# Kernel tuning notes

Measured on AMD Instinct MI355X. Metric: run time of the kernel, lower is better.

The kernel has to match this reference:

```python
import jax, jax.numpy as jnp
import numpy as np

K_MASK = -2.3819763e38  # gemma masking constant


def apply_rope(inputs, positions, head_dim):
    # inputs: [B, T, N, H], positions: [B, T]
    half = head_dim // 2
    fraction = 2.0 * jnp.arange(half, dtype=jnp.float32) / head_dim
    timescale = 10000.0 ** fraction                      # [half]
    sinusoid = positions[..., None].astype(jnp.float32) / timescale  # [B, T, half]
    sin = jnp.sin(sinusoid)[:, :, None, :]               # [B, T, 1, half]
    cos = jnp.cos(sinusoid)[:, :, None, :]
    first, second = jnp.split(inputs, 2, axis=-1)
    out = jnp.concatenate([first * cos - second * sin,
                           second * cos + first * sin], axis=-1)
    return out.astype(inputs.dtype)


def setup_inputs() -> dict:
    key = jax.random.key(0)
    k0, k1, k2, k3 = jax.random.split(key, 4)
    B, T, D, N, H = 4, 1024, 2048, 16, 128
    x = jax.random.normal(k0, (B, T, D), dtype=jnp.float32)
    wq = jax.random.normal(k1, (N, D, H), dtype=jnp.float32) * 0.02
    wkv = jax.random.normal(k2, (2, 1, D, H), dtype=jnp.float32) * 0.02  # MQA: 1 kv head
    wo = jax.random.normal(k3, (N, H, D), dtype=jnp.float32) * 0.02
    segment_pos = jnp.broadcast_to(jnp.arange(T, dtype=jnp.int32), (B, T))
    attn_mask = jnp.broadcast_to(jnp.tril(jnp.ones((T, T), dtype=bool)), (B, T, T))
    return {"x": x, "wq": wq, "wkv": wkv, "wo": wo,
            "segment_pos": segment_pos, "attn_mask": attn_mask}


def reference(x, wq, wkv, wo, segment_pos, attn_mask):
    N, _, H = wq.shape
    # projections
    q = jnp.einsum('BTD,NDH->BTNH', x, wq)          # [B,T,N,H]
    kv = jnp.einsum('BSD,CKDH->CBSKH', x, wkv)      # [2,B,S,1,H]
    k, v = kv[0], kv[1]
    # RoPE + scaling
    q = apply_rope(q, segment_pos, H) * (H ** -0.5)
    k = apply_rope(k, segment_pos, H)
    # MQA head repeat: 1 kv head -> N heads
    k = jnp.repeat(k, N, axis=-2)                   # [B,S,N,H]
    v = jnp.repeat(v, N, axis=-2)
    # attention with manual masked softmax
    logits = jnp.einsum('BTNH,BSNH->BTNS', q, k)
    padded = jnp.where(attn_mask[:, :, None, :], logits, K_MASK)
    probs = jax.nn.softmax(padded, axis=-1).astype(k.dtype)
    encoded = jnp.einsum('BTNS,BSNH->BTNH', probs, v)
    return jnp.einsum('BTNH,NHD->BTD', encoded, wo)
```

## Files before the change

kernel.cpp:

```cpp
#include <hip/hip_runtime.h>
#include <cstdint>
#include <cstddef>

typedef unsigned short u16;
typedef __attribute__((ext_vector_type(8))) short bf16x8;
typedef __attribute__((ext_vector_type(4))) float f32x4;

#define B_ 4
#define T_ 1024
#define D_ 2048
#define N_ 16
#define H_ 128
#define BT_ (B_ * T_)
#define KMASK (-2.3819763e38f)

__device__ __forceinline__ u16 f2bf(float f) {
  uint32_t u = __builtin_bit_cast(uint32_t, f);
  u += 0x7FFFu + ((u >> 16) & 1u);
  return (u16)(u >> 16);
}
__device__ __forceinline__ float bf2f(uint32_t u) {
  return __builtin_bit_cast(float, u << 16);
}

__device__ __forceinline__ void gload16(const void* g, void* l) {
  __builtin_amdgcn_global_load_lds((const __attribute__((address_space(1))) void*)g,
                                   (__attribute__((address_space(3))) void*)l, 16, 0, 0);
}

__global__ __launch_bounds__(256) void convert_x_kernel(const float* __restrict__ x,
                                                        u16* __restrict__ xb) {
  int i = (blockIdx.x * 256 + threadIdx.x) * 8;
  float4 v0 = *(const float4*)(x + i);
  float4 v1 = *(const float4*)(x + i + 4);
  uint4 o;
  o.x = (uint32_t)f2bf(v0.x) | ((uint32_t)f2bf(v0.y) << 16);
  o.y = (uint32_t)f2bf(v0.z) | ((uint32_t)f2bf(v0.w) << 16);
  o.z = (uint32_t)f2bf(v1.x) | ((uint32_t)f2bf(v1.y) << 16);
  o.w = (uint32_t)f2bf(v1.z) | ((uint32_t)f2bf(v1.w) << 16);
  *(uint4*)(xb + i) = o;
}

__global__ __launch_bounds__(256) void transpose_kernel(const float* __restrict__ src,
                                                        u16* __restrict__ dst, int R, int C) {
  __shared__ float tile[32][33];
  const int z = blockIdx.z;
  const float* s = src + (size_t)z * R * C;
  u16* d = dst + (size_t)z * R * C;
  const int tx = threadIdx.x, ty = threadIdx.y;
  const int r0 = blockIdx.y * 32, c0 = blockIdx.x * 32;
#pragma unroll
  for (int i = 0; i < 4; ++i)
    tile[ty + i * 8][tx] = s[(size_t)(r0 + ty + i * 8) * C + (c0 + tx)];
  __syncthreads();
#pragma unroll
  for (int i = 0; i < 4; ++i)
    d[(size_t)(c0 + ty + i * 8) * R + (r0 + tx)] = f2bf(tile[tx][ty + i * 8]);
}

__global__ __launch_bounds__(256) void rope_table_kernel(float* __restrict__ costab,
                                                         float* __restrict__ sintab) {
  int idx = blockIdx.x * 256 + threadIdx.x;
  int p = idx >> 6, i = idx & 63;
  float ts = powf(10000.0f, (float)i * (1.0f / 64.0f));
  float ang = (float)p / ts;
  costab[idx] = cosf(ang);
  sintab[idx] = sinf(ang);
}

__global__ __launch_bounds__(256) void proj_gemm_kernel(
    const u16* __restrict__ xb, const u16* __restrict__ wqT, const u16* __restrict__ wkvT,
    u16* __restrict__ qraw, u16* __restrict__ kraw, u16* __restrict__ vT) {
  __shared__ alignas(16) u16 a_lds[128 * 64];
  __shared__ alignas(16) u16 b_lds[128 * 64];
  const int bid = blockIdx.x;
  const int newbid = (bid & 7) * 72 + (bid >> 3);
  const int y = newbid >> 5;
  const int m0 = (newbid & 31) * 128;
  const u16* Bt = (y < N_) ? (wqT + (size_t)y * H_ * D_) : (wkvT + (size_t)(y - N_) * H_ * D_);
  const int tid = threadIdx.x;
  const int w = tid >> 6, lane = tid & 63;
  const int g = lane >> 4, li = lane & 15;
  const int mrow = (w >> 1) * 64, wc = (w & 1) * 64;
  f32x4 acc[4][4];
#pragma unroll
  for (int i = 0; i < 4; ++i)
#pragma unroll
    for (int j = 0; j < 4; ++j) acc[i][j] = (f32x4){0.f, 0.f, 0.f, 0.f};

  for (int k0 = 0; k0 < D_; k0 += 64) {
    __syncthreads();
#pragma unroll
    for (int it = 0; it < 4; ++it) {
      int chunk = it * 256 + tid;
      int row = chunk >> 3, cu = chunk & 7;
      gload16(xb + (size_t)(m0 + row) * D_ + k0 + ((cu ^ (row & 7)) << 3), &a_lds[chunk * 8]);
    }
#pragma unroll
    for (int it = 0; it < 4; ++it) {
      int chunk = it * 256 + tid;
      int row = chunk >> 3, cu = chunk & 7;
      gload16(Bt + (size_t)row * D_ + k0 + ((cu ^ (row & 7)) << 3), &b_lds[chunk * 8]);
    }
    __syncthreads();
#pragma unroll
    for (int c2 = 0; c2 < 2; ++c2) {
      bf16x8 af[4], bfr[4];
#pragma unroll
      for (int i = 0; i < 4; ++i) {
        int row = mrow + i * 16 + li;
        af[i] = *(const bf16x8*)((const char*)a_lds +
                                 row * 128 + ((c2 * 64 + g * 16) ^ ((row & 7) << 4)));
      }
#pragma unroll
      for (int j = 0; j < 4; ++j) {
        int row = wc + j * 16 + li;
        bfr[j] = *(const bf16x8*)((const char*)b_lds +
                                  row * 128 + ((c2 * 64 + g * 16) ^ ((row & 7) << 4)));
      }
#pragma unroll
      for (int i = 0; i < 4; ++i)
#pragma unroll
        for (int j = 0; j < 4; ++j)
          acc[i][j] = __builtin_amdgcn_mfma_f32_16x16x32_bf16(af[i], bfr[j], acc[i][j], 0, 0, 0);
    }
  }

  const int b = m0 >> 10;
  if (y == N_ + 1) {
    const int tbase0 = (m0 & 1023) + mrow;
#pragma unroll
    for (int i = 0; i < 4; ++i) {
      int tbase = tbase0 + i * 16 + g * 4;
#pragma unroll
      for (int j = 0; j < 4; ++j) {
        int h = wc + j * 16 + li;
        ushort4 pk;
        pk.x = f2bf(acc[i][j][0]);
        pk.y = f2bf(acc[i][j][1]);
        pk.z = f2bf(acc[i][j][2]);
        pk.w = f2bf(acc[i][j][3]);
        *(ushort4*)(vT + ((size_t)(b * H_ + h)) * T_ + tbase) = pk;
      }
    }
  } else {
    size_t rowbase = (y < N_) ? ((size_t)(b * N_ + y) * T_ + (m0 & 1023)) : (size_t)m0;
    u16* dst0 = (y < N_) ? qraw : kraw;
#pragma unroll
    for (int i = 0; i < 4; ++i)
#pragma unroll
      for (int r = 0; r < 4; ++r) {
        int trow = mrow + i * 16 + g * 4 + r;
        u16* dst = dst0 + (rowbase + trow) * H_;
#pragma unroll
        for (int j = 0; j < 4; ++j) dst[wc + j * 16 + li] = f2bf(acc[i][j][r]);
      }
  }
}

__global__ __launch_bounds__(256) void rope_apply_kernel(
    const u16* __restrict__ qraw, const u16* __restrict__ kraw,
    const int* __restrict__ segment_pos, const float* __restrict__ costab,
    const float* __restrict__ sintab, u16* __restrict__ qb, u16* __restrict__ kb) {
  const int rid = blockIdx.x * 8 + (threadIdx.x >> 5);
  const int j = threadIdx.x & 31;
  const u16* src;
  u16* dst;
  int bt;
  float scale;
  if (rid < BT_ * N_) {
    src = qraw + (size_t)rid * H_;
    dst = qb + (size_t)rid * H_;
    int t = rid & (T_ - 1);
    int b = rid >> 14;
    bt = b * T_ + t;
    scale = 0.08838834764831845f;
  } else {
    int r2 = rid - BT_ * N_;
    src = kraw + (size_t)r2 * H_;
    dst = kb + (size_t)r2 * H_;
    bt = r2;
    scale = 1.0f;
  }
  int p = segment_pos[bt];
  p = p < 0 ? 0 : (p > 1023 ? 1023 : p);
  uint32_t ua = *(const uint32_t*)(src + 2 * j);
  uint32_t ub = *(const uint32_t*)(src + 64 + 2 * j);
  float2 cv = *(const float2*)(costab + p * 64 + 2 * j);
  float2 sv = *(const float2*)(sintab + p * 64 + 2 * j);
  float f1a = bf2f(ua & 0xffffu), f1b = bf2f(ua >> 16);
  float f2a = bf2f(ub & 0xffffu), f2b = bf2f(ub >> 16);
  float o1a = (f1a * cv.x - f2a * sv.x) * scale;
  float o1b = (f1b * cv.y - f2b * sv.y) * scale;
  float o2a = (f2a * cv.x + f1a * sv.x) * scale;
  float o2b = (f2b * cv.y + f1b * sv.y) * scale;
  *(uint32_t*)(dst + 2 * j) = (uint32_t)f2bf(o1a) | ((uint32_t)f2bf(o1b) << 16);
  *(uint32_t*)(dst + 64 + 2 * j) = (uint32_t)f2bf(o2a) | ((uint32_t)f2bf(o2b) << 16);
}

__global__ __launch_bounds__(256) void attn_kernel(const u16* __restrict__ qb,
                                                   const u16* __restrict__ kb,
                                                   const u16* __restrict__ vT,
                                                   u16* __restrict__ enc) {
  __shared__ alignas(16) u16 k_lds[2][64 * 128];
  __shared__ alignas(16) u16 v_lds[2][128 * 64];
  __shared__ alignas(16) u16 p_lds[4 * 16 * 64];
  const int qt = (int)(gridDim.x - 1 - blockIdx.x);
  const int bn = blockIdx.y;
  const int b = bn >> 4, n = bn & 15;
  const int tid = threadIdx.x, w = tid >> 6, lane = tid & 63;
  const int g = lane >> 4, li = lane & 15;
  const int t0 = qt * 64 + w * 16;
  char* pbase = (char*)p_lds + w * 2048;

  bf16x8 qf[4];
  {
    const u16* qrow = qb + ((size_t)(b * N_ + n) * T_ + (t0 + li)) * H_;
#pragma unroll
    for (int c = 0; c < 4; ++c) qf[c] = *(const bf16x8*)(qrow + c * 32 + g * 8);
  }
  f32x4 o[8];
#pragma unroll
  for (int j = 0; j < 8; ++j) o[j] = (f32x4){0.f, 0.f, 0.f, 0.f};
  float m = -3e38f, lsum = 0.f;

  auto stageKV = [&](int buf, int s0) {
#pragma unroll
    for (int it = 0; it < 4; ++it) {
      int chunk = it * 256 + tid;
      int row = chunk >> 4, cu = chunk & 15;
      gload16(kb + ((size_t)b * T_ + s0 + row) * H_ + ((cu ^ (row & 7)) << 3),
              &k_lds[buf][chunk * 8]);
    }
#pragma unroll
    for (int it = 0; it < 4; ++it) {
      int chunk = it * 256 + tid;
      int row = chunk >> 3, cu = chunk & 7;
      gload16(vT + ((size_t)(b * H_ + row)) * T_ + s0 + ((cu ^ (row & 7)) << 3),
              &v_lds[buf][chunk * 8]);
    }
  };

  stageKV(0, 0);
  __syncthreads();
  int cur = 0;
  for (int st = 0; st <= qt; ++st) {
    if (st < qt) stageKV(cur ^ 1, (st + 1) * 64);

    f32x4 sacc[4];
#pragma unroll
    for (int fn = 0; fn < 4; ++fn) sacc[fn] = (f32x4){0.f, 0.f, 0.f, 0.f};
#pragma unroll
    for (int c = 0; c < 4; ++c)
#pragma unroll
      for (int fn = 0; fn < 4; ++fn) {
        int row = fn * 16 + li;
        bf16x8 kf = *(const bf16x8*)((const char*)&k_lds[cur][0] +
                                     row * 256 + ((c * 64 + g * 16) ^ ((row & 7) << 4)));
        sacc[fn] = __builtin_amdgcn_mfma_f32_16x16x32_bf16(kf, qf[c], sacc[fn], 0, 0, 0);
      }

    if (st == qt) {
#pragma unroll
      for (int fn = 0; fn < 4; ++fn)
#pragma unroll
        for (int r = 0; r < 4; ++r)
          if (fn * 16 + g * 4 + r > w * 16 + li) sacc[fn][r] = KMASK;
    }

    float mx = -3e38f;
#pragma unroll
    for (int fn = 0; fn < 4; ++fn)
#pragma unroll
      for (int r = 0; r < 4; ++r) mx = fmaxf(mx, sacc[fn][r]);
    mx = fmaxf(mx, __shfl_xor(mx, 16, 64));
    mx = fmaxf(mx, __shfl_xor(mx, 32, 64));
    float mn = fmaxf(m, mx);
    float alpha = __expf(m - mn);
    m = mn;
    float ps = 0.f;
#pragma unroll
    for (int fn = 0; fn < 4; ++fn)
#pragma unroll
      for (int r = 0; r < 4; ++r) {
        float p = __expf(sacc[fn][r] - mn);
        sacc[fn][r] = p;
        ps += p;
      }
    ps += __shfl_xor(ps, 16, 64);
    ps += __shfl_xor(ps, 32, 64);
    lsum = lsum * alpha + ps;

#pragma unroll
    for (int fn = 0; fn < 4; ++fn) {
      ushort4 pk;
      pk.x = f2bf(sacc[fn][0]);
      pk.y = f2bf(sacc[fn][1]);
      pk.z = f2bf(sacc[fn][2]);
      pk.w = f2bf(sacc[fn][3]);
      *(ushort4*)(pbase + li * 128 + ((fn * 32 + g * 8) ^ ((li & 7) << 4))) = pk;
    }

#pragma unroll
    for (int r = 0; r < 4; ++r) {
      float ar = __shfl(alpha, g * 4 + r, 64);
#pragma unroll
      for (int hn = 0; hn < 8; ++hn) o[hn][r] *= ar;
    }

#pragma unroll
    for (int c2 = 0; c2 < 2; ++c2) {
      bf16x8 pf = *(const bf16x8*)(pbase + li * 128 + ((c2 * 64 + g * 16) ^ ((li & 7) << 4)));
#pragma unroll
      for (int hn = 0; hn < 8; ++hn) {
        int hrow = hn * 16 + li;
        bf16x8 vf = *(const bf16x8*)((const char*)&v_lds[cur][0] +
                                     hrow * 128 + ((c2 * 64 + g * 16) ^ ((li & 7) << 4)));
        o[hn] = __builtin_amdgcn_mfma_f32_16x16x32_bf16(pf, vf, o[hn], 0, 0, 0);
      }
    }
    __syncthreads();
    cur ^= 1;
  }

#pragma unroll
  for (int r = 0; r < 4; ++r) {
    float lr = __shfl(lsum, g * 4 + r, 64);
    float inv = 1.0f / lr;
    int t = qt * 64 + w * 16 + g * 4 + r;
    u16* dst = enc + ((size_t)(b * T_ + t)) * (N_ * H_) + n * H_;
#pragma unroll
    for (int hn = 0; hn < 8; ++hn) dst[hn * 16 + li] = f2bf(o[hn][r] * inv);
  }
}

__global__ __launch_bounds__(256) void out_gemm_kernel(const u16* __restrict__ enc,
                                                       const u16* __restrict__ woT,
                                                       float* __restrict__ out) {
  __shared__ alignas(16) u16 a_lds[128 * 64];
  __shared__ alignas(16) u16 b_lds[128 * 64];
  const int bid = blockIdx.x;
  const int newbid = (bid & 7) * 64 + (bid >> 3);
  const int m0 = (newbid & 31) * 128;
  const int n0 = (newbid >> 5) * 128;
  const int tid = threadIdx.x, w = tid >> 6, lane = tid & 63;
  const int g = lane >> 4, li = lane & 15;
  const int mrow = (w >> 1) * 64, wc = (w & 1) * 64;
  f32x4 acc[4][4];
#pragma unroll
  for (int i = 0; i < 4; ++i)
#pragma unroll
    for (int j = 0; j < 4; ++j) acc[i][j] = (f32x4){0.f, 0.f, 0.f, 0.f};

  for (int k0 = 0; k0 < D_; k0 += 64) {
    __syncthreads();
#pragma unroll
    for (int it = 0; it < 4; ++it) {
      int chunk = it * 256 + tid;
      int row = chunk >> 3, cu = chunk & 7;
      gload16(enc + (size_t)(m0 + row) * D_ + k0 + ((cu ^ (row & 7)) << 3), &a_lds[chunk * 8]);
    }
#pragma unroll
    for (int it = 0; it < 4; ++it) {
      int chunk = it * 256 + tid;
      int row = chunk >> 3, cu = chunk & 7;
      gload16(woT + (size_t)(n0 + row) * D_ + k0 + ((cu ^ (row & 7)) << 3), &b_lds[chunk * 8]);
    }
    __syncthreads();
#pragma unroll
    for (int c2 = 0; c2 < 2; ++c2) {
      bf16x8 af[4], bfr[4];
#pragma unroll
      for (int i = 0; i < 4; ++i) {
        int row = mrow + i * 16 + li;
        af[i] = *(const bf16x8*)((const char*)a_lds +
                                 row * 128 + ((c2 * 64 + g * 16) ^ ((row & 7) << 4)));
      }
#pragma unroll
      for (int j = 0; j < 4; ++j) {
        int row = wc + j * 16 + li;
        bfr[j] = *(const bf16x8*)((const char*)b_lds +
                                  row * 128 + ((c2 * 64 + g * 16) ^ ((row & 7) << 4)));
      }
#pragma unroll
      for (int i = 0; i < 4; ++i)
#pragma unroll
        for (int j = 0; j < 4; ++j)
          acc[i][j] = __builtin_amdgcn_mfma_f32_16x16x32_bf16(af[i], bfr[j], acc[i][j], 0, 0, 0);
    }
  }
#pragma unroll
  for (int i = 0; i < 4; ++i)
#pragma unroll
    for (int r = 0; r < 4; ++r) {
      int bt = m0 + mrow + i * 16 + g * 4 + r;
      float* dst = out + (size_t)bt * D_ + n0 + wc;
#pragma unroll
      for (int j = 0; j < 4; ++j) dst[j * 16 + li] = acc[i][j][r];
    }
}

extern "C" void kernel_launch(void* const* d_in, const int* in_sizes, int n_in,
                              void* d_out, int out_size, void* d_ws, size_t ws_size,
                              hipStream_t stream) {
  const float* x = (const float*)d_in[0];
  const float* wq = (const float*)d_in[1];
  const float* wkv = (const float*)d_in[2];
  const float* wo = (const float*)d_in[3];
  const int* segment_pos = (const int*)d_in[4];
  float* out = (float*)d_out;

  char* ws = (char*)d_ws;
  size_t off = 0;
  auto alloc = [&](size_t bytes) -> void* {
    void* p = ws + off;
    off += (bytes + 255) & ~(size_t)255;
    return p;
  };
  u16* xb   = (u16*)alloc((size_t)BT_ * D_ * 2);
  u16* wqT  = (u16*)alloc((size_t)N_ * H_ * D_ * 2);
  u16* wkvT = (u16*)alloc((size_t)2 * H_ * D_ * 2);
  u16* woT  = (u16*)alloc((size_t)D_ * N_ * H_ * 2);
  u16* qb   = (u16*)alloc((size_t)B_ * N_ * T_ * H_ * 2);
  u16* kb   = (u16*)alloc((size_t)B_ * T_ * H_ * 2);
  u16* kraw = (u16*)alloc((size_t)B_ * T_ * H_ * 2);
  u16* vT   = (u16*)alloc((size_t)B_ * H_ * T_ * 2);
  u16* enc  = (u16*)alloc((size_t)BT_ * N_ * H_ * 2);
  float* costab = (float*)alloc(1024 * 64 * 4);
  float* sintab = (float*)alloc(1024 * 64 * 4);
  u16* qraw = enc;

  convert_x_kernel<<<BT_ * D_ / 8 / 256, 256, 0, stream>>>(x, xb);
  dim3 tb(32, 8);
  transpose_kernel<<<dim3(H_ / 32, D_ / 32, N_), tb, 0, stream>>>(wq, wqT, D_, H_);
  transpose_kernel<<<dim3(H_ / 32, D_ / 32, 2), tb, 0, stream>>>(wkv, wkvT, D_, H_);
  transpose_kernel<<<dim3(D_ / 32, D_ / 32, 1), tb, 0, stream>>>(wo, woT, N_ * H_, D_);
  rope_table_kernel<<<256, 256, 0, stream>>>(costab, sintab);
  proj_gemm_kernel<<<576, 256, 0, stream>>>(xb, wqT, wkvT, qraw, kraw, vT);
  rope_apply_kernel<<<(BT_ * N_ + BT_) / 8, 256, 0, stream>>>(qraw, kraw, segment_pos,
                                                              costab, sintab, qb, kb);
  attn_kernel<<<dim3(T_ / 64, B_ * N_), 256, 0, stream>>>(qb, kb, vT, enc);
  out_gemm_kernel<<<512, 256, 0, stream>>>(enc, woT, out);
}
```

Before: 203.1 us.

## Fuse Q RoPE into attention, widen query tile, read V directly from global

Q RoPE and scaling now happen inside the attention kernel on the register fragments, so the separate pass over the full Q tensor (write then reread) goes away and only K still gets a standalone RoPE kernel. Each attention block now covers 128 query rows, with each wave handling 32 rows, so every staged K tile feeds twice as many MFMAs. V fragments are loaded straight from global memory instead of through LDS, and waves skip key tiles that lie entirely above their causal diagonal. It also adds setprio around the MFMA sections and a 1D grid ordered so the largest causal tiles launch first. The tradeoffs are higher register pressure, uncoalesced V reads, and fewer blocks in flight.

```diff
diff --git a/kernel.cpp b/kernel.cpp
--- a/kernel.cpp
+++ b/kernel.cpp
@@ -158,31 +158,15 @@
   }
 }
 
-__global__ __launch_bounds__(256) void rope_apply_kernel(
-    const u16* __restrict__ qraw, const u16* __restrict__ kraw,
-    const int* __restrict__ segment_pos, const float* __restrict__ costab,
-    const float* __restrict__ sintab, u16* __restrict__ qb, u16* __restrict__ kb) {
+__global__ __launch_bounds__(256) void rope_apply_k_kernel(
+    const u16* __restrict__ kraw, const int* __restrict__ segment_pos,
+    const float* __restrict__ costab, const float* __restrict__ sintab,
+    u16* __restrict__ kb) {
   const int rid = blockIdx.x * 8 + (threadIdx.x >> 5);
   const int j = threadIdx.x & 31;
-  const u16* src;
-  u16* dst;
-  int bt;
-  float scale;
-  if (rid < BT_ * N_) {
-    src = qraw + (size_t)rid * H_;
-    dst = qb + (size_t)rid * H_;
-    int t = rid & (T_ - 1);
-    int b = rid >> 14;
-    bt = b * T_ + t;
-    scale = 0.08838834764831845f;
-  } else {
-    int r2 = rid - BT_ * N_;
-    src = kraw + (size_t)r2 * H_;
-    dst = kb + (size_t)r2 * H_;
-    bt = r2;
-    scale = 1.0f;
-  }
-  int p = segment_pos[bt];
+  const u16* src = kraw + (size_t)rid * H_;
+  u16* dst = kb + (size_t)rid * H_;
+  int p = segment_pos[rid];
   p = p < 0 ? 0 : (p > 1023 ? 1023 : p);
   uint32_t ua = *(const uint32_t*)(src + 2 * j);
   uint32_t ub = *(const uint32_t*)(src + 64 + 2 * j);
@@ -190,41 +174,63 @@
   float2 sv = *(const float2*)(sintab + p * 64 + 2 * j);
   float f1a = bf2f(ua & 0xffffu), f1b = bf2f(ua >> 16);
   float f2a = bf2f(ub & 0xffffu), f2b = bf2f(ub >> 16);
-  float o1a = (f1a * cv.x - f2a * sv.x) * scale;
-  float o1b = (f1b * cv.y - f2b * sv.y) * scale;
-  float o2a = (f2a * cv.x + f1a * sv.x) * scale;
-  float o2b = (f2b * cv.y + f1b * sv.y) * scale;
-  *(uint32_t*)(dst + 2 * j) = (uint32_t)f2bf(o1a) | ((uint32_t)f2bf(o1b) << 16);
-  *(uint32_t*)(dst + 64 + 2 * j) = (uint32_t)f2bf(o2a) | ((uint32_t)f2bf(o2b) << 16);
-}
-
-__global__ __launch_bounds__(256) void attn_kernel(const u16* __restrict__ qb,
-                                                   const u16* __restrict__ kb,
-                                                   const u16* __restrict__ vT,
-                                                   u16* __restrict__ enc) {
+  *(uint32_t*)(dst + 2 * j) =
+      (uint32_t)f2bf(f1a * cv.x - f2a * sv.x) | ((uint32_t)f2bf(f1b * cv.y - f2b * sv.y) << 16);
+  *(uint32_t*)(dst + 64 + 2 * j) =
+      (uint32_t)f2bf(f2a * cv.x + f1a * sv.x) | ((uint32_t)f2bf(f2b * cv.y + f1b * sv.y) << 16);
+}
+
+__global__ __launch_bounds__(256) void attn_kernel(
+    const u16* __restrict__ qraw, const u16* __restrict__ kb, const u16* __restrict__ vT,
+    const int* __restrict__ segment_pos, const float* __restrict__ costab,
+    const float* __restrict__ sintab, u16* __restrict__ enc) {
   __shared__ alignas(16) u16 k_lds[2][64 * 128];
-  __shared__ alignas(16) u16 v_lds[2][128 * 64];
-  __shared__ alignas(16) u16 p_lds[4 * 16 * 64];
-  const int qt = (int)(gridDim.x - 1 - blockIdx.x);
-  const int bn = blockIdx.y;
+  __shared__ alignas(16) u16 p_lds[4 * 32 * 64];
+  const int bx = blockIdx.x;
+  const int qt8 = 7 - (bx >> 6);
+  const int bn = bx & 63;
   const int b = bn >> 4, n = bn & 15;
   const int tid = threadIdx.x, w = tid >> 6, lane = tid & 63;
   const int g = lane >> 4, li = lane & 15;
-  const int t0 = qt * 64 + w * 16;
-  char* pbase = (char*)p_lds + w * 2048;
-
-  bf16x8 qf[4];
-  {
-    const u16* qrow = qb + ((size_t)(b * N_ + n) * T_ + (t0 + li)) * H_;
-#pragma unroll
-    for (int c = 0; c < 4; ++c) qf[c] = *(const bf16x8*)(qrow + c * 32 + g * 8);
+  const int t0w = qt8 * 128 + w * 32;
+  char* pbase = (char*)p_lds + w * 4096;
+
+  bf16x8 qf[2][4];
+  const float scale = 0.08838834764831845f;
+#pragma unroll
+  for (int i = 0; i < 2; ++i) {
+    const int trow = t0w + i * 16 + li;
+    const u16* qrow = qraw + ((size_t)(b * N_ + n) * T_ + trow) * H_;
+#pragma unroll
+    for (int c = 0; c < 4; ++c) qf[i][c] = *(const bf16x8*)(qrow + c * 32 + g * 8);
+    int p = segment_pos[b * T_ + trow];
+    p = p < 0 ? 0 : (p > 1023 ? 1023 : p);
+#pragma unroll
+    for (int c = 0; c < 2; ++c) {
+      const float* cp = costab + p * 64 + c * 32 + g * 8;
+      const float* sp = sintab + p * 64 + c * 32 + g * 8;
+      f32x4 cv0 = *(const f32x4*)cp, cv1 = *(const f32x4*)(cp + 4);
+      f32x4 sv0 = *(const f32x4*)sp, sv1 = *(const f32x4*)(sp + 4);
+#pragma unroll
+      for (int e = 0; e < 8; ++e) {
+        float cvv = e < 4 ? cv0[e] : cv1[e - 4];
+        float svv = e < 4 ? sv0[e] : sv1[e - 4];
+        float f1 = bf2f((u16)qf[i][c][e]);
+        float f2 = bf2f((u16)qf[i][c + 2][e]);
+        qf[i][c][e] = (short)f2bf((f1 * cvv - f2 * svv) * scale);
+        qf[i][c + 2][e] = (short)f2bf((f2 * cvv + f1 * svv) * scale);
+      }
+    }
   }
-  f32x4 o[8];
-#pragma unroll
-  for (int j = 0; j < 8; ++j) o[j] = (f32x4){0.f, 0.f, 0.f, 0.f};
-  float m = -3e38f, lsum = 0.f;
-
-  auto stageKV = [&](int buf, int s0) {
+
+  f32x4 o[2][8];
+#pragma unroll
+  for (int i = 0; i < 2; ++i)
+#pragma unroll
+    for (int hn = 0; hn < 8; ++hn) o[i][hn] = (f32x4){0.f, 0.f, 0.f, 0.f};
+  float m[2] = {-3e38f, -3e38f}, lsum[2] = {0.f, 0.f};
+
+  auto stageK = [&](int buf, int s0) {
 #pragma unroll
     for (int it = 0; it < 4; ++it) {
       int chunk = it * 256 + tid;
@@ -232,106 +238,126 @@
       gload16(kb + ((size_t)b * T_ + s0 + row) * H_ + ((cu ^ (row & 7)) << 3),
               &k_lds[buf][chunk * 8]);
     }
-#pragma unroll
-    for (int it = 0; it < 4; ++it) {
-      int chunk = it * 256 + tid;
-      int row = chunk >> 3, cu = chunk & 7;
-      gload16(vT + ((size_t)(b * H_ + row)) * T_ + s0 + ((cu ^ (row & 7)) << 3),
-              &v_lds[buf][chunk * 8]);
-    }
   };
 
-  stageKV(0, 0);
+  const int nst = 2 * (qt8 + 1);
+  stageK(0, 0);
   __syncthreads();
   int cur = 0;
-  for (int st = 0; st <= qt; ++st) {
-    if (st < qt) stageKV(cur ^ 1, (st + 1) * 64);
-
-    f32x4 sacc[4];
-#pragma unroll
-    for (int fn = 0; fn < 4; ++fn) sacc[fn] = (f32x4){0.f, 0.f, 0.f, 0.f};
-#pragma unroll
-    for (int c = 0; c < 4; ++c)
-#pragma unroll
-      for (int fn = 0; fn < 4; ++fn) {
-        int row = fn * 16 + li;
-        bf16x8 kf = *(const bf16x8*)((const char*)&k_lds[cur][0] +
-                                     row * 256 + ((c * 64 + g * 16) ^ ((row & 7) << 4)));
-        sacc[fn] = __builtin_amdgcn_mfma_f32_16x16x32_bf16(kf, qf[c], sacc[fn], 0, 0, 0);
-      }
-
-    if (st == qt) {
-#pragma unroll
-      for (int fn = 0; fn < 4; ++fn)
-#pragma unroll
-        for (int r = 0; r < 4; ++r)
-          if (fn * 16 + g * 4 + r > w * 16 + li) sacc[fn][r] = KMASK;
-    }
-
-    float mx = -3e38f;
-#pragma unroll
-    for (int fn = 0; fn < 4; ++fn)
-#pragma unroll
-      for (int r = 0; r < 4; ++r) mx = fmaxf(mx, sacc[fn][r]);
-    mx = fmaxf(mx, __shfl_xor(mx, 16, 64));
-    mx = fmaxf(mx, __shfl_xor(mx, 32, 64));
-    float mn = fmaxf(m, mx);
-    float alpha = __expf(m - mn);
-    m = mn;
-    float ps = 0.f;
-#pragma unroll
-    for (int fn = 0; fn < 4; ++fn)
-#pragma unroll
-      for (int r = 0; r < 4; ++r) {
-        float p = __expf(sacc[fn][r] - mn);
-        sacc[fn][r] = p;
-        ps += p;
-      }
-    ps += __shfl_xor(ps, 16, 64);
-    ps += __shfl_xor(ps, 32, 64);
-    lsum = lsum * alpha + ps;
-
-#pragma unroll
-    for (int fn = 0; fn < 4; ++fn) {
-      ushort4 pk;
-      pk.x = f2bf(sacc[fn][0]);
-      pk.y = f2bf(sacc[fn][1]);
-      pk.z = f2bf(sacc[fn][2]);
-      pk.w = f2bf(sacc[fn][3]);
-      *(ushort4*)(pbase + li * 128 + ((fn * 32 + g * 8) ^ ((li & 7) << 4))) = pk;
-    }
-
-#pragma unroll
-    for (int r = 0; r < 4; ++r) {
-      float ar = __shfl(alpha, g * 4 + r, 64);
-#pragma unroll
-      for (int hn = 0; hn < 8; ++hn) o[hn][r] *= ar;
-    }
-
-#pragma unroll
-    for (int c2 = 0; c2 < 2; ++c2) {
-      bf16x8 pf = *(const bf16x8*)(pbase + li * 128 + ((c2 * 64 + g * 16) ^ ((li & 7) << 4)));
-#pragma unroll
-      for (int hn = 0; hn < 8; ++hn) {
-        int hrow = hn * 16 + li;
-        bf16x8 vf = *(const bf16x8*)((const char*)&v_lds[cur][0] +
-                                     hrow * 128 + ((c2 * 64 + g * 16) ^ ((li & 7) << 4)));
-        o[hn] = __builtin_amdgcn_mfma_f32_16x16x32_bf16(pf, vf, o[hn], 0, 0, 0);
-      }
+  for (int st = 0; st < nst; ++st) {
+    const int s0 = st * 64;
+    if (st + 1 < nst) stageK(cur ^ 1, (st + 1) * 64);
+    if (s0 <= t0w + 31) {
+      bf16x8 vf[2][8];
+#pragma unroll
+      for (int c2 = 0; c2 < 2; ++c2)
+#pragma unroll
+        for (int hn = 0; hn < 8; ++hn)
+          vf[c2][hn] =
+              *(const bf16x8*)(vT + ((size_t)(b * H_ + hn * 16 + li)) * T_ + s0 + c2 * 32 + g * 8);
+
+      f32x4 sacc[2][4];
+#pragma unroll
+      for (int i = 0; i < 2; ++i)
+#pragma unroll
+        for (int fn = 0; fn < 4; ++fn) sacc[i][fn] = (f32x4){0.f, 0.f, 0.f, 0.f};
+      __builtin_amdgcn_s_setprio(1);
+#pragma unroll
+      for (int c = 0; c < 4; ++c) {
+        bf16x8 kf[4];
+#pragma unroll
+        for (int fn = 0; fn < 4; ++fn) {
+          int row = fn * 16 + li;
+          kf[fn] = *(const bf16x8*)((const char*)&k_lds[cur][0] +
+                                    row * 256 + ((c * 64 + g * 16) ^ ((row & 7) << 4)));
+        }
+#pragma unroll
+        for (int i = 0; i < 2; ++i)
+#pragma unroll
+          for (int fn = 0; fn < 4; ++fn)
+            sacc[i][fn] = __builtin_amdgcn_mfma_f32_16x16x32_bf16(kf[fn], qf[i][c],
+                                                                  sacc[i][fn], 0, 0, 0);
+      }
+      __builtin_amdgcn_s_setprio(0);
+
+      const bool needmask = (s0 + 63 > t0w);
+#pragma unroll
+      for (int i = 0; i < 2; ++i) {
+        if (needmask) {
+          int trow = t0w + i * 16 + li;
+#pragma unroll
+          for (int fn = 0; fn < 4; ++fn)
+#pragma unroll
+            for (int r = 0; r < 4; ++r)
+              if (s0 + fn * 16 + g * 4 + r > trow) sacc[i][fn][r] = KMASK;
+        }
+        float mx = -3e38f;
+#pragma unroll
+        for (int fn = 0; fn < 4; ++fn)
+#pragma unroll
+          for (int r = 0; r < 4; ++r) mx = fmaxf(mx, sacc[i][fn][r]);
+        mx = fmaxf(mx, __shfl_xor(mx, 16, 64));
+        mx = fmaxf(mx, __shfl_xor(mx, 32, 64));
+        float mn = fmaxf(m[i], mx);
+        float alpha = __expf(m[i] - mn);
+        m[i] = mn;
+        float ps = 0.f;
+#pragma unroll
+        for (int fn = 0; fn < 4; ++fn)
+#pragma unroll
+          for (int r = 0; r < 4; ++r) {
+            float p = __expf(sacc[i][fn][r] - mn);
+            sacc[i][fn][r] = p;
+            ps += p;
+          }
+        ps += __shfl_xor(ps, 16, 64);
+        ps += __shfl_xor(ps, 32, 64);
+        lsum[i] = lsum[i] * alpha + ps;
+#pragma unroll
+        for (int fn = 0; fn < 4; ++fn) {
+          ushort4 pk;
+          pk.x = f2bf(sacc[i][fn][0]);
+          pk.y = f2bf(sacc[i][fn][1]);
+          pk.z = f2bf(sacc[i][fn][2]);
+          pk.w = f2bf(sacc[i][fn][3]);
+          *(ushort4*)(pbase + (i * 16 + li) * 128 + ((fn * 32 + g * 8) ^ ((li & 7) << 4))) = pk;
+        }
+#pragma unroll
+        for (int r = 0; r < 4; ++r) {
+          float ar = __shfl(alpha, g * 4 + r, 64);
+#pragma unroll
+          for (int hn = 0; hn < 8; ++hn) o[i][hn][r] *= ar;
+        }
+      }
+
+      __builtin_amdgcn_s_setprio(1);
+#pragma unroll
+      for (int i = 0; i < 2; ++i)
+#pragma unroll
+        for (int c2 = 0; c2 < 2; ++c2) {
+          bf16x8 pf = *(const bf16x8*)(pbase + (i * 16 + li) * 128 +
+                                       ((c2 * 64 + g * 16) ^ ((li & 7) << 4)));
+#pragma unroll
+          for (int hn = 0; hn < 8; ++hn)
+            o[i][hn] = __builtin_amdgcn_mfma_f32_16x16x32_bf16(pf, vf[c2][hn], o[i][hn], 0, 0, 0);
+        }
+      __builtin_amdgcn_s_setprio(0);
     }
     __syncthreads();
     cur ^= 1;
   }
 
 #pragma unroll
-  for (int r = 0; r < 4; ++r) {
-    float lr = __shfl(lsum, g * 4 + r, 64);
-    float inv = 1.0f / lr;
-    int t = qt * 64 + w * 16 + g * 4 + r;
-    u16* dst = enc + ((size_t)(b * T_ + t)) * (N_ * H_) + n * H_;
-#pragma unroll
-    for (int hn = 0; hn < 8; ++hn) dst[hn * 16 + li] = f2bf(o[hn][r] * inv);
-  }
+  for (int i = 0; i < 2; ++i)
+#pragma unroll
+    for (int r = 0; r < 4; ++r) {
+      float lr = __shfl(lsum[i], g * 4 + r, 64);
+      float inv = 1.0f / lr;
+      int t = t0w + i * 16 + g * 4 + r;
+      u16* dst = enc + ((size_t)(b * T_ + t)) * (N_ * H_) + n * H_;
+#pragma unroll
+      for (int hn = 0; hn < 8; ++hn) dst[hn * 16 + li] = f2bf(o[i][hn][r] * inv);
+    }
 }
 
 __global__ __launch_bounds__(256) void out_gemm_kernel(const u16* __restrict__ enc,
@@ -421,14 +447,13 @@
   u16* wqT  = (u16*)alloc((size_t)N_ * H_ * D_ * 2);
   u16* wkvT = (u16*)alloc((size_t)2 * H_ * D_ * 2);
   u16* woT  = (u16*)alloc((size_t)D_ * N_ * H_ * 2);
-  u16* qb   = (u16*)alloc((size_t)B_ * N_ * T_ * H_ * 2);
+  u16* qraw = (u16*)alloc((size_t)B_ * N_ * T_ * H_ * 2);
   u16* kb   = (u16*)alloc((size_t)B_ * T_ * H_ * 2);
   u16* kraw = (u16*)alloc((size_t)B_ * T_ * H_ * 2);
   u16* vT   = (u16*)alloc((size_t)B_ * H_ * T_ * 2);
   u16* enc  = (u16*)alloc((size_t)BT_ * N_ * H_ * 2);
   float* costab = (float*)alloc(1024 * 64 * 4);
   float* sintab = (float*)alloc(1024 * 64 * 4);
-  u16* qraw = enc;
 
   convert_x_kernel<<<BT_ * D_ / 8 / 256, 256, 0, stream>>>(x, xb);
   dim3 tb(32, 8);
@@ -437,8 +462,7 @@
   transpose_kernel<<<dim3(D_ / 32, D_ / 32, 1), tb, 0, stream>>>(wo, woT, N_ * H_, D_);
   rope_table_kernel<<<256, 256, 0, stream>>>(costab, sintab);
   proj_gemm_kernel<<<576, 256, 0, stream>>>(xb, wqT, wkvT, qraw, kraw, vT);
-  rope_apply_kernel<<<(BT_ * N_ + BT_) / 8, 256, 0, stream>>>(qraw, kraw, segment_pos,
-                                                              costab, sintab, qb, kb);
-  attn_kernel<<<dim3(T_ / 64, B_ * N_), 256, 0, stream>>>(qb, kb, vT, enc);
+  rope_apply_k_kernel<<<BT_ / 8, 256, 0, stream>>>(kraw, segment_pos, costab, sintab, kb);
+  attn_kernel<<<512, 256, 0, stream>>>(qraw, kb, vT, segment_pos, costab, sintab, enc);
   out_gemm_kernel<<<512, 256, 0, stream>>>(enc, woT, out);
 }
```

Measured after the change: 211.4 us. 4.1% more time.
